# Kernel tuning notes

Measured on AMD Instinct MI355X. Metric: run time of the kernel, lower is better.

The kernel has to match this reference:

```python
import jax, jax.numpy as jnp
import numpy as np

C, NX, NY, P = 64, 1024, 1024, 100000  # num_bev_features, grid x, grid y, num pillars


def setup_inputs() -> dict:
    key = jax.random.key(0)
    k1, k2 = jax.random.split(key)
    pillar_features = jax.random.normal(k1, (C, P), dtype=jnp.float32)
    # unique BEV cells for each pillar (real pillars occupy distinct grid cells)
    flat = jax.random.permutation(k2, NX * NY)[:P]
    y = (flat // NX).astype(jnp.int32)
    x = (flat % NX).astype(jnp.int32)
    z = jnp.zeros_like(x)  # coords[:, :, 0]; nz == 1 so this column is 0
    coords = jnp.stack([z, y, x], axis=-1)[None]  # [1, P, 3] int32
    return {"pillar_features": pillar_features, "coords": coords}


def reference(pillar_features, coords):
    # indices = coords[:,:,0] + coords[:,:,1]*nx + coords[:,:,2]  -> flat BEV index per pillar
    idx = coords[0, :, 0] + coords[0, :, 1] * NX + coords[0, :, 2]  # [P]
    # scatter pillar features into zero-initialized dense grid (same index for all channels,
    # replacing the wasteful ones-matmul broadcast in the torch code)
    spatial = jnp.zeros((C, NY * NX), dtype=pillar_features.dtype)
    spatial = spatial.at[:, idx].set(pillar_features)
    return spatial.reshape(1, C, NY, NX)
```

## Files before the change

### kernel.cpp

```cpp
#include <hip/hip_runtime.h>
#include <hip/hip_bf16.h>


constexpr int C_CH   = 64;
constexpr int NX_G   = 1024;
constexpr int NY_G   = 1024;
constexpr int NCELLS = NX_G * NY_G;
constexpr int QUADS  = NCELLS / 4;
constexpr int CPT    = 8;
constexpr int GROUPS = C_CH / CPT;

typedef __attribute__((ext_vector_type(4))) float f32x4;

__global__ void pp_fill_map(int4* __restrict__ map) {
    int t = blockIdx.x * blockDim.x + threadIdx.x;
    map[t] = make_int4(-1, -1, -1, -1);
}

__global__ void pp_build_map(const int* __restrict__ coords,
                             int* __restrict__ map, int P) {
    int p = blockIdx.x * blockDim.x + threadIdx.x;
    if (p >= P) return;
    int z = coords[3 * p + 0];
    int y = coords[3 * p + 1];
    int x = coords[3 * p + 2];
    map[z + y * NX_G + x] = p;
}

__global__ __launch_bounds__(256)
void pp_gather(const float* __restrict__ pf,
               const int* __restrict__ map,
               float* __restrict__ out, int P) {
    int t = blockIdx.x * blockDim.x + threadIdx.x;
    int q = t & (QUADS - 1);
    int g = t >> 18;
    const int4 pid = reinterpret_cast<const int4*>(map)[q];
    const int cbase = g * CPT;

    f32x4 v[CPT];
#pragma unroll
    for (int i = 0; i < CPT; ++i) {
        const float* __restrict__ pfc = pf + (size_t)(cbase + i) * P;
        v[i].x = (pid.x >= 0) ? pfc[pid.x] : 0.0f;
        v[i].y = (pid.y >= 0) ? pfc[pid.y] : 0.0f;
        v[i].z = (pid.z >= 0) ? pfc[pid.z] : 0.0f;
        v[i].w = (pid.w >= 0) ? pfc[pid.w] : 0.0f;
    }
#pragma unroll
    for (int i = 0; i < CPT; ++i) {
        f32x4* dst = reinterpret_cast<f32x4*>(out + (size_t)(cbase + i) * NCELLS) + q;
        __builtin_nontemporal_store(v[i], dst);
    }
}

extern "C" void kernel_launch(void* const* d_in, const int* in_sizes, int n_in,
                              void* d_out, int out_size, void* d_ws, size_t ws_size,
                              hipStream_t stream) {
    const float* pf     = (const float*)d_in[0];
    const int*   coords = (const int*)d_in[1];
    float*       out    = (float*)d_out;
    int*         map    = (int*)d_ws;

    const int P = in_sizes[0] / C_CH;

    pp_fill_map<<<QUADS / 256, 256, 0, stream>>>((int4*)map);
    pp_build_map<<<(P + 255) / 256, 256, 0, stream>>>(coords, map, P);

    const int threads = GROUPS * QUADS;
    pp_gather<<<threads / 256, 256, 0, stream>>>(pf, map, out, P);
}
```

Baseline: 87.55 us.

## Transpose pillar features to pillar-major and gather float4 per pillar

```diff
diff --git a/kernel.cpp b/kernel.cpp
--- a/kernel.cpp
+++ b/kernel.cpp
@@ -7,8 +7,7 @@
 constexpr int NY_G   = 1024;
 constexpr int NCELLS = NX_G * NY_G;
 constexpr int QUADS  = NCELLS / 4;
-constexpr int CPT    = 8;
-constexpr int GROUPS = C_CH / CPT;
+constexpr int GROUPS = 16;
 
 typedef __attribute__((ext_vector_type(4))) float f32x4;
 
@@ -17,39 +16,66 @@
     map[t] = make_int4(-1, -1, -1, -1);
 }
 
-__global__ void pp_build_map(const int* __restrict__ coords,
-                             int* __restrict__ map, int P) {
-    int p = blockIdx.x * blockDim.x + threadIdx.x;
-    if (p >= P) return;
-    int z = coords[3 * p + 0];
-    int y = coords[3 * p + 1];
-    int x = coords[3 * p + 2];
-    map[z + y * NX_G + x] = p;
+__global__ __launch_bounds__(256)
+void pp_transpose_buildmap(const float* __restrict__ pf,
+                           const int* __restrict__ coords,
+                           float* __restrict__ pfT,
+                           int* __restrict__ map, int P) {
+    __shared__ float tile[64][65];
+    const int pbase = blockIdx.x * 64;
+    const int lane  = threadIdx.x & 63;
+    const int row4  = threadIdx.x >> 6;
+    const int p     = pbase + lane;
+    const bool pin  = (p < P);
+
+#pragma unroll
+    for (int r = 0; r < 16; ++r) {
+        int c = (r << 2) + row4;
+        tile[c][lane] = pin ? pf[(size_t)c * P + p] : 0.0f;
+    }
+
+    if (threadIdx.x < 64 && pin) {
+        int z = coords[3 * p + 0];
+        int y = coords[3 * p + 1];
+        int x = coords[3 * p + 2];
+        map[z + y * NX_G + x] = p;
+    }
+    __syncthreads();
+
+    const int j  = threadIdx.x >> 2;
+    const int c0 = (threadIdx.x & 3) << 4;
+    if (pbase + j < P) {
+        float* dst = pfT + (size_t)(pbase + j) * 64 + c0;
+#pragma unroll
+        for (int k = 0; k < 16; k += 4) {
+            f32x4 v = { tile[c0 + k][j], tile[c0 + k + 1][j],
+                        tile[c0 + k + 2][j], tile[c0 + k + 3][j] };
+            *reinterpret_cast<f32x4*>(dst + k) = v;
+        }
+    }
 }
 
 __global__ __launch_bounds__(256)
-void pp_gather(const float* __restrict__ pf,
+void pp_gather(const float* __restrict__ pfT,
                const int* __restrict__ map,
-               float* __restrict__ out, int P) {
+               float* __restrict__ out) {
     int t = blockIdx.x * blockDim.x + threadIdx.x;
     int q = t & (QUADS - 1);
     int g = t >> 18;
     const int4 pid = reinterpret_cast<const int4*>(map)[q];
-    const int cbase = g * CPT;
+    const int c0 = g << 2;
 
-    f32x4 v[CPT];
+    f32x4 a = {0,0,0,0}, b = {0,0,0,0}, c = {0,0,0,0}, d = {0,0,0,0};
+    if (pid.x >= 0) a = *reinterpret_cast<const f32x4*>(pfT + ((size_t)pid.x << 6) + c0);
+    if (pid.y >= 0) b = *reinterpret_cast<const f32x4*>(pfT + ((size_t)pid.y << 6) + c0);
+    if (pid.z >= 0) c = *reinterpret_cast<const f32x4*>(pfT + ((size_t)pid.z << 6) + c0);
+    if (pid.w >= 0) d = *reinterpret_cast<const f32x4*>(pfT + ((size_t)pid.w << 6) + c0);
+
 #pragma unroll
-    for (int i = 0; i < CPT; ++i) {
-        const float* __restrict__ pfc = pf + (size_t)(cbase + i) * P;
-        v[i].x = (pid.x >= 0) ? pfc[pid.x] : 0.0f;
-        v[i].y = (pid.y >= 0) ? pfc[pid.y] : 0.0f;
-        v[i].z = (pid.z >= 0) ? pfc[pid.z] : 0.0f;
-        v[i].w = (pid.w >= 0) ? pfc[pid.w] : 0.0f;
-    }
-#pragma unroll
-    for (int i = 0; i < CPT; ++i) {
-        f32x4* dst = reinterpret_cast<f32x4*>(out + (size_t)(cbase + i) * NCELLS) + q;
-        __builtin_nontemporal_store(v[i], dst);
+    for (int i = 0; i < 4; ++i) {
+        f32x4 v = { a[i], b[i], c[i], d[i] };
+        f32x4* dst = reinterpret_cast<f32x4*>(out + (size_t)(c0 + i) * NCELLS) + q;
+        __builtin_nontemporal_store(v, dst);
     }
 }
 
@@ -60,12 +86,15 @@
     const int*   coords = (const int*)d_in[1];
     float*       out    = (float*)d_out;
     int*         map    = (int*)d_ws;
+    float*       pfT    = (float*)((char*)d_ws + (size_t)NCELLS * sizeof(int));
 
     const int P = in_sizes[0] / C_CH;
 
     pp_fill_map<<<QUADS / 256, 256, 0, stream>>>((int4*)map);
-    pp_build_map<<<(P + 255) / 256, 256, 0, stream>>>(coords, map, P);
+
+    const int tblocks = (P + 63) / 64;
+    pp_transpose_buildmap<<<tblocks, 256, 0, stream>>>(pf, coords, pfT, map, P);
 
     const int threads = GROUPS * QUADS;
-    pp_gather<<<threads / 256, 256, 0, stream>>>(pf, map, out, P);
+    pp_gather<<<threads / 256, 256, 0, stream>>>(pfT, map, out);
 }
```

New measurement: 72.35 us, median of 2. 17.4% less time.
